# Kernel optimization log

Measured on AMD Instinct MI355X. Metric: run time of the kernel, lower is better.

The kernel has to match this reference:

```python
import jax, jax.numpy as jnp
import numpy as np

B, R, T, N = 32, 2, 128, 128
C_IN, C_OUT = 64, 64


def setup_inputs() -> dict:
    key = jax.random.key(0)
    k1, k2, k3 = jax.random.split(key, 3)
    x = jax.random.normal(k1, (B, C_IN, T, N), dtype=jnp.float32)
    # non-negative adjacency weights (degrees stay positive after +I)
    A = jax.random.uniform(k2, (B, R, T, N, N), dtype=jnp.float32)
    # 1x1 conv weight (out_channels*relation, in_channels) and bias
    W = jax.random.normal(k3, (R * C_OUT, C_IN), dtype=jnp.float32) * 0.02
    b = jnp.zeros((R * C_OUT,), dtype=jnp.float32)
    return {"x": x, "A": A, "W": W, "b": b}


def _normalized_laplacian_tilde(A):
    # A: (..., N, N). GCN-style: A~ = A + I, D~^{-1/2} A~ D~^{-1/2}
    n = A.shape[-1]
    A_t = A + jnp.eye(n, dtype=A.dtype)
    d = jax.lax.rsqrt(A_t.sum(axis=-1))  # (..., N)
    return A_t * d[..., :, None] * d[..., None, :]


def reference(x, A, W, b):
    # 1x1 Conv2d over (T, N): pointwise channel mix
    y = jnp.einsum('bctn,oc->botn', x, W) + b[None, :, None, None]
    y = y.reshape(B, R, C_OUT, T, N)
    # drop_edge is identity in eval mode; normalize each (b, r, t) adjacency
    A_norm = _normalized_laplacian_tilde(A)  # (B, R, T, N, N)
    # torch.bmm(x_r[:, :, t, :], A_rt_norm) summed over relations:
    # x_out[b,c,t,n] = sum_r sum_m y[b,r,c,t,m] * A_norm[b,r,t,m,n]
    x_out = jnp.einsum('brctm,brtmn->bctn', y, A_norm)
    return (x_out, A)
```

## Files before the change

### kernel.cpp

```cpp
#include <hip/hip_runtime.h>
#include <hip/hip_bf16.h>

#define TB 512

constexpr size_t XOUT_ELEMS = 32ull * 64 * 128 * 128;

typedef short bf16x8  __attribute__((ext_vector_type(8)));
typedef short short4v __attribute__((ext_vector_type(4)));
typedef float f32x4   __attribute__((ext_vector_type(4)));

static __device__ __forceinline__ short f2bf(float f) {
    __hip_bfloat16 hb = __float2bfloat16(f);
    return *reinterpret_cast<short*>(&hb);
}


__global__ __launch_bounds__(TB, 4)
void gcn_fused(const float* __restrict__ xg, const float* __restrict__ Ag,
               const float* __restrict__ Wg, const float* __restrict__ bg,
               float* __restrict__ outg)
{
    __shared__ float4 smem4[5120];
    char*  smem = (char*)smem4;
    float* dd   = (float*)smem;

    const int tid = threadIdx.x;
    const int w   = tid >> 6;
    const int l   = tid & 63;
    const int g   = l >> 5;
    const int h   = l & 31;
    const int l15 = l & 15;
    const int l4  = l >> 4;

    const int blk = blockIdx.x;
    const int b = blk >> 7, t = blk & 127;

    {
        float vv[4][4];
        #pragma unroll
        for (int i = 0; i < 4; ++i) {
            int c = 8*w + 4*g + i;
            f32x4 v = __builtin_nontemporal_load(
                (const f32x4*)(xg + ((size_t)(b*64 + c)*128 + t)*128 + 4*h));
            vv[i][0] = v[0]; vv[i][1] = v[1]; vv[i][2] = v[2]; vv[i][3] = v[3];
        }
        int po = w ^ (h & 7);
        #pragma unroll
        for (int e = 0; e < 4; ++e) {
            int n = 4*h + e;
            short4v pk;
            pk[0] = f2bf(vv[0][e]); pk[1] = f2bf(vv[1][e]);
            pk[2] = f2bf(vv[2][e]); pk[3] = f2bf(vv[3][e]);
            *(short4v*)(smem + n*128 + po*16 + 8*g) = pk;
        }
    }
    #pragma unroll
    for (int k2 = 0; k2 < 4; ++k2) {
        int q = tid + TB*k2;
        f32x4 v = ((const f32x4*)Wg)[q];
        int o = q >> 4, oct = (q >> 1) & 7, hf = q & 1;
        short4v pk;
        pk[0] = f2bf(v[0]); pk[1] = f2bf(v[1]); pk[2] = f2bf(v[2]); pk[3] = f2bf(v[3]);
        *(short4v*)(smem + 49152 + o*128 + (oct ^ (o & 7))*16 + hf*8) = pk;
    }
    float bia[8];
    #pragma unroll
    for (int ot = 0; ot < 8; ++ot) bia[ot] = bg[16*ot + l15];
    __syncthreads();

    {
        const int n    = 16*w + l15;
        const int keyx = (n >> 2) & 7;
        bf16x8 af0 = *(const bf16x8*)(smem + n*128 + ((0 + l4) ^ keyx)*16);
        bf16x8 af1 = *(const bf16x8*)(smem + n*128 + ((4 + l4) ^ keyx)*16);
        const int m0   = 16*w + 4*l4;
        const int pob  = m0 >> 3;
        const int keyw = l15 & 7;
        #pragma unroll
        for (int ot = 0; ot < 8; ++ot) {
            int o = 16*ot + l15;
            f32x4 acc = {0.f, 0.f, 0.f, 0.f};
            bf16x8 bf0 = *(const bf16x8*)(smem + 49152 + o*128 + ((0 + l4) ^ keyw)*16);
            bf16x8 bf1 = *(const bf16x8*)(smem + 49152 + o*128 + ((4 + l4) ^ keyw)*16);
            acc = __builtin_amdgcn_mfma_f32_16x16x32_bf16(af0, bf0, acc, 0, 0, 0);
            acc = __builtin_amdgcn_mfma_f32_16x16x32_bf16(af1, bf1, acc, 0, 0, 0);
            short4v pk;
            pk[0] = f2bf(acc[0] + bia[ot]); pk[1] = f2bf(acc[1] + bia[ot]);
            pk[2] = f2bf(acc[2] + bia[ot]); pk[3] = f2bf(acc[3] + bia[ot]);
            int po = pob ^ (o & 7);
            *(short4v*)(smem + 16384 + o*256 + po*16 + (m0 & 7)*2) = pk;
        }
    }
    __syncthreads();

    f32x4 tot[4] = {{0,0,0,0},{0,0,0,0},{0,0,0,0},{0,0,0,0}};

    #pragma unroll 1
    for (int r = 0; r < 2; ++r) {
        const size_t aoff = ((size_t)(b*2 + r)*128 + t) * 16384;
        const float* gA = Ag + aoff;
        float*       gO = outg + XOUT_ELEMS + aoff;

        {
            float vv[2][4][4];
            #pragma unroll
            for (int k = 0; k < 2; ++k)
                #pragma unroll
                for (int i = 0; i < 4; ++i) {
                    int m = 16*w + 8*k + 4*g + i;
                    f32x4 v = __builtin_nontemporal_load((const f32x4*)(gA + m*128 + 4*h));
                    __builtin_nontemporal_store(v, (f32x4*)(gO + m*128 + 4*h));
                    vv[k][i][0] = v[0]; vv[k][i][1] = v[1];
                    vv[k][i][2] = v[2]; vv[k][i][3] = v[3];
                }
            #pragma unroll
            for (int k = 0; k < 2; ++k)
                #pragma unroll
                for (int i = 0; i < 4; ++i) {
                    float s = vv[k][i][0] + vv[k][i][1] + vv[k][i][2] + vv[k][i][3];
                    s += __shfl_xor(s, 16); s += __shfl_xor(s, 8);
                    s += __shfl_xor(s, 4);  s += __shfl_xor(s, 2); s += __shfl_xor(s, 1);
                    float dv = rsqrtf(1.0f + s);
                    if (h == 4*w + 2*k + g) vv[k][i][i] += 1.0f;
                    vv[k][i][0] *= dv; vv[k][i][1] *= dv;
                    vv[k][i][2] *= dv; vv[k][i][3] *= dv;
                    if (h == 0) dd[16*w + 8*k + 4*g + i] = dv;
                }
            #pragma unroll
            for (int k = 0; k < 2; ++k) {
                int po = (2*w + k) ^ (h & 7);
                #pragma unroll
                for (int e = 0; e < 4; ++e) {
                    int n = 4*h + e;
                    short4v pk;
                    pk[0] = f2bf(vv[k][0][e]); pk[1] = f2bf(vv[k][1][e]);
                    pk[2] = f2bf(vv[k][2][e]); pk[3] = f2bf(vv[k][3][e]);
                    *(short4v*)(smem + 49152 + n*256 + po*16 + 8*g) = pk;
                }
            }
        }
        __syncthreads();

        {
            f32x4 acc[4] = {{0,0,0,0},{0,0,0,0},{0,0,0,0},{0,0,0,0}};
            const int n    = 16*w + l15;
            const int keyA = (n >> 2) & 7;
            #pragma unroll
            for (int s = 0; s < 4; ++s) {
                int octk = 4*s + l4;
                bf16x8 bfr = *(const bf16x8*)(smem + 49152 + n*256 + (octk ^ keyA)*16);
                #pragma unroll
                for (int ct = 0; ct < 4; ++ct) {
                    int o  = 64*r + 16*ct + l15;
                    bf16x8 afr = *(const bf16x8*)(smem + 16384 + o*256 + (octk ^ (o & 7))*16);
                    acc[ct] = __builtin_amdgcn_mfma_f32_16x16x32_bf16(afr, bfr, acc[ct], 0, 0, 0);
                }
            }
            float dn = dd[n];
            #pragma unroll
            for (int ct = 0; ct < 4; ++ct)
                #pragma unroll
                for (int j = 0; j < 4; ++j) tot[ct][j] += acc[ct][j] * dn;
        }
        __syncthreads();
    }

    #pragma unroll
    for (int ct = 0; ct < 4; ++ct)
        #pragma unroll
        for (int j = 0; j < 4; ++j) {
            int c = 16*ct + 4*l4 + j;
            int n = 16*w + l15;
            __builtin_nontemporal_store(tot[ct][j],
                &outg[((size_t)(b*64 + c)*128 + t)*128 + n]);
        }
}

extern "C" void kernel_launch(void* const* d_in, const int* in_sizes, int n_in,
                              void* d_out, int out_size, void* d_ws, size_t ws_size,
                              hipStream_t stream) {
    const float* x    = (const float*)d_in[0];
    const float* A    = (const float*)d_in[1];
    const float* W    = (const float*)d_in[2];
    const float* bias = (const float*)d_in[3];
    float* out = (float*)d_out;

    dim3 grid(32 * 128);
    dim3 block(TB);
    hipLaunchKernelGGL(gcn_fused, grid, block, 0, stream, x, A, W, bias, out);
}
```

Before: 236.4 us.

## Prefetch A tiles into registers and overlap loads with GEMM stages

Issues the global loads for x, W and the first adjacency slice together at kernel start, and prefetches the second relation's adjacency slice before the first relation's GEMM. Replaces __syncthreads with an LDS-only waitcnt plus s_barrier so outstanding global loads are not drained at each barrier. The relation loop is unrolled into explicit stages, and A/x loads drop the nontemporal hint. This is meant to hide global memory latency behind LDS work and MFMA, at the cost of higher register pressure under the 4-block launch bound.

```diff
diff --git a/kernel.cpp b/kernel.cpp
--- a/kernel.cpp
+++ b/kernel.cpp
@@ -14,6 +14,73 @@
     return *reinterpret_cast<short*>(&hb);
 }
 
+static __device__ __forceinline__ void lgkm_barrier() {
+    asm volatile("s_waitcnt lgkmcnt(0)" ::: "memory");
+    __builtin_amdgcn_s_barrier();
+    asm volatile("" ::: "memory");
+}
+
+
+static __device__ __forceinline__ void process_A(f32x4 (&av)[2][4], float* __restrict__ gO,
+                                                 char* smem, float* dd,
+                                                 int w, int g, int h) {
+    #pragma unroll
+    for (int k = 0; k < 2; ++k)
+        #pragma unroll
+        for (int i = 0; i < 4; ++i) {
+            int m = 16*w + 8*k + 4*g + i;
+            __builtin_nontemporal_store(av[k][i], (f32x4*)(gO + m*128 + 4*h));
+        }
+    #pragma unroll
+    for (int k = 0; k < 2; ++k)
+        #pragma unroll
+        for (int i = 0; i < 4; ++i) {
+            float s = av[k][i][0] + av[k][i][1] + av[k][i][2] + av[k][i][3];
+            s += __shfl_xor(s, 16); s += __shfl_xor(s, 8);
+            s += __shfl_xor(s, 4);  s += __shfl_xor(s, 2); s += __shfl_xor(s, 1);
+            float dv = rsqrtf(1.0f + s);
+            if (h == 4*w + 2*k + g) av[k][i][i] += 1.0f;
+            av[k][i][0] *= dv; av[k][i][1] *= dv;
+            av[k][i][2] *= dv; av[k][i][3] *= dv;
+            if (h == 0) dd[16*w + 8*k + 4*g + i] = dv;
+        }
+    #pragma unroll
+    for (int k = 0; k < 2; ++k) {
+        int po = (2*w + k) ^ (h & 7);
+        #pragma unroll
+        for (int e = 0; e < 4; ++e) {
+            int n = 4*h + e;
+            short4v pk;
+            pk[0] = f2bf(av[k][0][e]); pk[1] = f2bf(av[k][1][e]);
+            pk[2] = f2bf(av[k][2][e]); pk[3] = f2bf(av[k][3][e]);
+            *(short4v*)(smem + 49152 + n*256 + po*16 + 8*g) = pk;
+        }
+    }
+}
+
+static __device__ __forceinline__ void gemm2(int r, f32x4 (&tot)[4],
+                                             const char* smem, const float* dd,
+                                             int l15, int l4, int w) {
+    f32x4 acc[4] = {{0,0,0,0},{0,0,0,0},{0,0,0,0},{0,0,0,0}};
+    const int n    = 16*w + l15;
+    const int keyA = (n >> 2) & 7;
+    #pragma unroll
+    for (int s = 0; s < 4; ++s) {
+        int octk = 4*s + l4;
+        bf16x8 bfr = *(const bf16x8*)(smem + 49152 + n*256 + (octk ^ keyA)*16);
+        #pragma unroll
+        for (int ct = 0; ct < 4; ++ct) {
+            int o  = 64*r + 16*ct + l15;
+            bf16x8 afr = *(const bf16x8*)(smem + 16384 + o*256 + (octk ^ (o & 7))*16);
+            acc[ct] = __builtin_amdgcn_mfma_f32_16x16x32_bf16(afr, bfr, acc[ct], 0, 0, 0);
+        }
+    }
+    float dn = dd[n];
+    #pragma unroll
+    for (int ct = 0; ct < 4; ++ct)
+        #pragma unroll
+        for (int j = 0; j < 4; ++j) tot[ct][j] += acc[ct][j] * dn;
+}
 
 __global__ __launch_bounds__(TB, 4)
 void gcn_fused(const float* __restrict__ xg, const float* __restrict__ Ag,
@@ -35,38 +102,55 @@
     const int blk = blockIdx.x;
     const int b = blk >> 7, t = blk & 127;
 
+    const size_t aoff0 = ((size_t)(b*2 + 0)*128 + t) * 16384;
+    const size_t aoff1 = ((size_t)(b*2 + 1)*128 + t) * 16384;
+    const float* gA0 = Ag + aoff0;
+    const float* gA1 = Ag + aoff1;
+    float*       gO0 = outg + XOUT_ELEMS + aoff0;
+    float*       gO1 = outg + XOUT_ELEMS + aoff1;
+
+    f32x4 xr[4];
+    #pragma unroll
+    for (int i = 0; i < 4; ++i) {
+        int c = 8*w + 4*g + i;
+        xr[i] = *(const f32x4*)(xg + ((size_t)(b*64 + c)*128 + t)*128 + 4*h);
+    }
+    f32x4 wr[4];
+    #pragma unroll
+    for (int k2 = 0; k2 < 4; ++k2) wr[k2] = ((const f32x4*)Wg)[tid + TB*k2];
+    f32x4 av[2][4];
+    #pragma unroll
+    for (int k = 0; k < 2; ++k)
+        #pragma unroll
+        for (int i = 0; i < 4; ++i) {
+            int m = 16*w + 8*k + 4*g + i;
+            av[k][i] = *(const f32x4*)(gA0 + m*128 + 4*h);
+        }
+    float bia[8];
+    #pragma unroll
+    for (int ot = 0; ot < 8; ++ot) bia[ot] = bg[16*ot + l15];
+
     {
-        float vv[4][4];
-        #pragma unroll
-        for (int i = 0; i < 4; ++i) {
-            int c = 8*w + 4*g + i;
-            f32x4 v = __builtin_nontemporal_load(
-                (const f32x4*)(xg + ((size_t)(b*64 + c)*128 + t)*128 + 4*h));
-            vv[i][0] = v[0]; vv[i][1] = v[1]; vv[i][2] = v[2]; vv[i][3] = v[3];
-        }
         int po = w ^ (h & 7);
         #pragma unroll
         for (int e = 0; e < 4; ++e) {
             int n = 4*h + e;
             short4v pk;
-            pk[0] = f2bf(vv[0][e]); pk[1] = f2bf(vv[1][e]);
-            pk[2] = f2bf(vv[2][e]); pk[3] = f2bf(vv[3][e]);
+            pk[0] = f2bf(xr[0][e]); pk[1] = f2bf(xr[1][e]);
+            pk[2] = f2bf(xr[2][e]); pk[3] = f2bf(xr[3][e]);
             *(short4v*)(smem + n*128 + po*16 + 8*g) = pk;
         }
     }
     #pragma unroll
     for (int k2 = 0; k2 < 4; ++k2) {
         int q = tid + TB*k2;
-        f32x4 v = ((const f32x4*)Wg)[q];
         int o = q >> 4, oct = (q >> 1) & 7, hf = q & 1;
         short4v pk;
-        pk[0] = f2bf(v[0]); pk[1] = f2bf(v[1]); pk[2] = f2bf(v[2]); pk[3] = f2bf(v[3]);
+        pk[0] = f2bf(wr[k2][0]); pk[1] = f2bf(wr[k2][1]);
+        pk[2] = f2bf(wr[k2][2]); pk[3] = f2bf(wr[k2][3]);
         *(short4v*)(smem + 49152 + o*128 + (oct ^ (o & 7))*16 + hf*8) = pk;
     }
-    float bia[8];
-    #pragma unroll
-    for (int ot = 0; ot < 8; ++ot) bia[ot] = bg[16*ot + l15];
-    __syncthreads();
+    lgkm_barrier();
 
     {
         const int n    = 16*w + l15;
@@ -91,79 +175,25 @@
             *(short4v*)(smem + 16384 + o*256 + po*16 + (m0 & 7)*2) = pk;
         }
     }
-    __syncthreads();
+    lgkm_barrier();
 
     f32x4 tot[4] = {{0,0,0,0},{0,0,0,0},{0,0,0,0},{0,0,0,0}};
 
-    #pragma unroll 1
-    for (int r = 0; r < 2; ++r) {
-        const size_t aoff = ((size_t)(b*2 + r)*128 + t) * 16384;
-        const float* gA = Ag + aoff;
-        float*       gO = outg + XOUT_ELEMS + aoff;
-
-        {
-            float vv[2][4][4];
-            #pragma unroll
-            for (int k = 0; k < 2; ++k)
-                #pragma unroll
-                for (int i = 0; i < 4; ++i) {
-                    int m = 16*w + 8*k + 4*g + i;
-                    f32x4 v = __builtin_nontemporal_load((const f32x4*)(gA + m*128 + 4*h));
-                    __builtin_nontemporal_store(v, (f32x4*)(gO + m*128 + 4*h));
-                    vv[k][i][0] = v[0]; vv[k][i][1] = v[1];
-                    vv[k][i][2] = v[2]; vv[k][i][3] = v[3];
-                }
-            #pragma unroll
-            for (int k = 0; k < 2; ++k)
-                #pragma unroll
-                for (int i = 0; i < 4; ++i) {
-                    float s = vv[k][i][0] + vv[k][i][1] + vv[k][i][2] + vv[k][i][3];
-                    s += __shfl_xor(s, 16); s += __shfl_xor(s, 8);
-                    s += __shfl_xor(s, 4);  s += __shfl_xor(s, 2); s += __shfl_xor(s, 1);
-                    float dv = rsqrtf(1.0f + s);
-                    if (h == 4*w + 2*k + g) vv[k][i][i] += 1.0f;
-                    vv[k][i][0] *= dv; vv[k][i][1] *= dv;
-                    vv[k][i][2] *= dv; vv[k][i][3] *= dv;
-                    if (h == 0) dd[16*w + 8*k + 4*g + i] = dv;
-                }
-            #pragma unroll
-            for (int k = 0; k < 2; ++k) {
-                int po = (2*w + k) ^ (h & 7);
-                #pragma unroll
-                for (int e = 0; e < 4; ++e) {
-                    int n = 4*h + e;
-                    short4v pk;
-                    pk[0] = f2bf(vv[k][0][e]); pk[1] = f2bf(vv[k][1][e]);
-                    pk[2] = f2bf(vv[k][2][e]); pk[3] = f2bf(vv[k][3][e]);
-                    *(short4v*)(smem + 49152 + n*256 + po*16 + 8*g) = pk;
-                }
-            }
-        }
-        __syncthreads();
-
-        {
-            f32x4 acc[4] = {{0,0,0,0},{0,0,0,0},{0,0,0,0},{0,0,0,0}};
-            const int n    = 16*w + l15;
-            const int keyA = (n >> 2) & 7;
-            #pragma unroll
-            for (int s = 0; s < 4; ++s) {
-                int octk = 4*s + l4;
-                bf16x8 bfr = *(const bf16x8*)(smem + 49152 + n*256 + (octk ^ keyA)*16);
-                #pragma unroll
-                for (int ct = 0; ct < 4; ++ct) {
-                    int o  = 64*r + 16*ct + l15;
-                    bf16x8 afr = *(const bf16x8*)(smem + 16384 + o*256 + (octk ^ (o & 7))*16);
-                    acc[ct] = __builtin_amdgcn_mfma_f32_16x16x32_bf16(afr, bfr, acc[ct], 0, 0, 0);
-                }
-            }
-            float dn = dd[n];
-            #pragma unroll
-            for (int ct = 0; ct < 4; ++ct)
-                #pragma unroll
-                for (int j = 0; j < 4; ++j) tot[ct][j] += acc[ct][j] * dn;
-        }
-        __syncthreads();
-    }
+    process_A(av, gO0, smem, dd, w, g, h);
+    #pragma unroll
+    for (int k = 0; k < 2; ++k)
+        #pragma unroll
+        for (int i = 0; i < 4; ++i) {
+            int m = 16*w + 8*k + 4*g + i;
+            av[k][i] = *(const f32x4*)(gA1 + m*128 + 4*h);
+        }
+    lgkm_barrier();
+    gemm2(0, tot, smem, dd, l15, l4, w);
+    lgkm_barrier();
+
+    process_A(av, gO1, smem, dd, w, g, h);
+    lgkm_barrier();
+    gemm2(1, tot, smem, dd, l15, l4, w);
 
     #pragma unroll
     for (int ct = 0; ct < 4; ++ct)
```

After: 260.4 us. 10.2% more time.

## Split adjacency staging into halves to shrink LDS and raise occupancy

Applied to the files above, without the earlier changes.

The per-relation adjacency tile is now staged and multiplied in two 64-row halves that reuse the x staging region. This cuts shared memory from about 80KB to about 48KB, and launch bounds are raised to target 6 blocks per CU. W and bias are no longer staged in LDS; each wave loads them straight from global memory and converts them to bf16 in registers. The cost is extra barriers per relation, redundant global W reads in every block, and possible register pressure under the tighter launch bound.

```diff
diff --git a/kernel.cpp b/kernel.cpp
--- a/kernel.cpp
+++ b/kernel.cpp
@@ -15,14 +15,66 @@
 }
 
 
-__global__ __launch_bounds__(TB, 4)
+static __device__ __forceinline__ void stage_half(const float* __restrict__ gA,
+                                                  float* __restrict__ gO, int hf,
+                                                  char* smem, float* dd,
+                                                  int w, int g, int h) {
+    const int mb = 64*hf + 8*w + 4*g;
+    f32x4 av[4];
+    #pragma unroll
+    for (int i = 0; i < 4; ++i)
+        av[i] = __builtin_nontemporal_load((const f32x4*)(gA + (size_t)(mb+i)*128 + 4*h));
+    #pragma unroll
+    for (int i = 0; i < 4; ++i)
+        __builtin_nontemporal_store(av[i], (f32x4*)(gO + (size_t)(mb+i)*128 + 4*h));
+    #pragma unroll
+    for (int i = 0; i < 4; ++i) {
+        float s = av[i][0] + av[i][1] + av[i][2] + av[i][3];
+        s += __shfl_xor(s, 16); s += __shfl_xor(s, 8);
+        s += __shfl_xor(s, 4);  s += __shfl_xor(s, 2); s += __shfl_xor(s, 1);
+        float dv = rsqrtf(1.0f + s);
+        if (h == 16*hf + 2*w + g) av[i][i] += 1.0f;
+        av[i][0] *= dv; av[i][1] *= dv; av[i][2] *= dv; av[i][3] *= dv;
+        if (h == 0) dd[mb + i] = dv;
+    }
+    const int po = w ^ (h & 7);
+    #pragma unroll
+    for (int e = 0; e < 4; ++e) {
+        int n = 4*h + e;
+        short4v pk;
+        pk[0] = f2bf(av[0][e]); pk[1] = f2bf(av[1][e]);
+        pk[2] = f2bf(av[2][e]); pk[3] = f2bf(av[3][e]);
+        *(short4v*)(smem + n*128 + po*16 + 8*g) = pk;
+    }
+}
+
+static __device__ __forceinline__ void gemm2_half(int r, int hf, f32x4 (&acc)[4],
+                                                  const char* smem,
+                                                  int l15, int l4, int w) {
+    const int n    = 16*w + l15;
+    const int keyA = (n >> 2) & 7;
+    #pragma unroll
+    for (int s = 0; s < 2; ++s) {
+        int ol = 4*s + l4;
+        bf16x8 bfr = *(const bf16x8*)(smem + n*128 + (ol ^ keyA)*16);
+        int og = 8*hf + 4*s + l4;
+        #pragma unroll
+        for (int ct = 0; ct < 4; ++ct) {
+            int o  = 64*r + 16*ct + l15;
+            bf16x8 afr = *(const bf16x8*)(smem + 16384 + o*256 + (og ^ (o & 7))*16);
+            acc[ct] = __builtin_amdgcn_mfma_f32_16x16x32_bf16(afr, bfr, acc[ct], 0, 0, 0);
+        }
+    }
+}
+
+__global__ __launch_bounds__(TB, 6)
 void gcn_fused(const float* __restrict__ xg, const float* __restrict__ Ag,
                const float* __restrict__ Wg, const float* __restrict__ bg,
                float* __restrict__ outg)
 {
-    __shared__ float4 smem4[5120];
+    __shared__ float4 smem4[3104];
     char*  smem = (char*)smem4;
-    float* dd   = (float*)smem;
+    float* dd   = (float*)(smem + 49152);
 
     const int tid = threadIdx.x;
     const int w   = tid >> 6;
@@ -36,36 +88,23 @@
     const int b = blk >> 7, t = blk & 127;
 
     {
-        float vv[4][4];
+        f32x4 xr[4];
         #pragma unroll
         for (int i = 0; i < 4; ++i) {
             int c = 8*w + 4*g + i;
-            f32x4 v = __builtin_nontemporal_load(
+            xr[i] = __builtin_nontemporal_load(
                 (const f32x4*)(xg + ((size_t)(b*64 + c)*128 + t)*128 + 4*h));
-            vv[i][0] = v[0]; vv[i][1] = v[1]; vv[i][2] = v[2]; vv[i][3] = v[3];
         }
         int po = w ^ (h & 7);
         #pragma unroll
         for (int e = 0; e < 4; ++e) {
             int n = 4*h + e;
             short4v pk;
-            pk[0] = f2bf(vv[0][e]); pk[1] = f2bf(vv[1][e]);
-            pk[2] = f2bf(vv[2][e]); pk[3] = f2bf(vv[3][e]);
+            pk[0] = f2bf(xr[0][e]); pk[1] = f2bf(xr[1][e]);
+            pk[2] = f2bf(xr[2][e]); pk[3] = f2bf(xr[3][e]);
             *(short4v*)(smem + n*128 + po*16 + 8*g) = pk;
         }
     }
-    #pragma unroll
-    for (int k2 = 0; k2 < 4; ++k2) {
-        int q = tid + TB*k2;
-        f32x4 v = ((const f32x4*)Wg)[q];
-        int o = q >> 4, oct = (q >> 1) & 7, hf = q & 1;
-        short4v pk;
-        pk[0] = f2bf(v[0]); pk[1] = f2bf(v[1]); pk[2] = f2bf(v[2]); pk[3] = f2bf(v[3]);
-        *(short4v*)(smem + 49152 + o*128 + (oct ^ (o & 7))*16 + hf*8) = pk;
-    }
-    float bia[8];
-    #pragma unroll
-    for (int ot = 0; ot < 8; ++ot) bia[ot] = bg[16*ot + l15];
     __syncthreads();
 
     {
@@ -73,20 +112,27 @@
         const int keyx = (n >> 2) & 7;
         bf16x8 af0 = *(const bf16x8*)(smem + n*128 + ((0 + l4) ^ keyx)*16);
         bf16x8 af1 = *(const bf16x8*)(smem + n*128 + ((4 + l4) ^ keyx)*16);
-        const int m0   = 16*w + 4*l4;
-        const int pob  = m0 >> 3;
-        const int keyw = l15 & 7;
+        const int m0  = 16*w + 4*l4;
+        const int pob = m0 >> 3;
         #pragma unroll
         for (int ot = 0; ot < 8; ++ot) {
             int o = 16*ot + l15;
+            const f32x4* wp = (const f32x4*)(Wg + o*64 + 8*l4);
+            f32x4 w0a = wp[0], w0b = wp[1];
+            const f32x4* wq = (const f32x4*)(Wg + o*64 + 32 + 8*l4);
+            f32x4 w1a = wq[0], w1b = wq[1];
+            float bb = bg[o];
+            bf16x8 bf0, bf1;
+            bf0[0]=f2bf(w0a[0]); bf0[1]=f2bf(w0a[1]); bf0[2]=f2bf(w0a[2]); bf0[3]=f2bf(w0a[3]);
+            bf0[4]=f2bf(w0b[0]); bf0[5]=f2bf(w0b[1]); bf0[6]=f2bf(w0b[2]); bf0[7]=f2bf(w0b[3]);
+            bf1[0]=f2bf(w1a[0]); bf1[1]=f2bf(w1a[1]); bf1[2]=f2bf(w1a[2]); bf1[3]=f2bf(w1a[3]);
+            bf1[4]=f2bf(w1b[0]); bf1[5]=f2bf(w1b[1]); bf1[6]=f2bf(w1b[2]); bf1[7]=f2bf(w1b[3]);
             f32x4 acc = {0.f, 0.f, 0.f, 0.f};
-            bf16x8 bf0 = *(const bf16x8*)(smem + 49152 + o*128 + ((0 + l4) ^ keyw)*16);
-            bf16x8 bf1 = *(const bf16x8*)(smem + 49152 + o*128 + ((4 + l4) ^ keyw)*16);
             acc = __builtin_amdgcn_mfma_f32_16x16x32_bf16(af0, bf0, acc, 0, 0, 0);
             acc = __builtin_amdgcn_mfma_f32_16x16x32_bf16(af1, bf1, acc, 0, 0, 0);
             short4v pk;
-            pk[0] = f2bf(acc[0] + bia[ot]); pk[1] = f2bf(acc[1] + bia[ot]);
-            pk[2] = f2bf(acc[2] + bia[ot]); pk[3] = f2bf(acc[3] + bia[ot]);
+            pk[0] = f2bf(acc[0] + bb); pk[1] = f2bf(acc[1] + bb);
+            pk[2] = f2bf(acc[2] + bb); pk[3] = f2bf(acc[3] + bb);
             int po = pob ^ (o & 7);
             *(short4v*)(smem + 16384 + o*256 + po*16 + (m0 & 7)*2) = pk;
         }
@@ -101,67 +147,21 @@
         const float* gA = Ag + aoff;
         float*       gO = outg + XOUT_ELEMS + aoff;
 
-        {
-            float vv[2][4][4];
+        f32x4 acc[4] = {{0,0,0,0},{0,0,0,0},{0,0,0,0},{0,0,0,0}};
+
+        stage_half(gA, gO, 0, smem, dd, w, g, h);
+        __syncthreads();
+        gemm2_half(r, 0, acc, smem, l15, l4, w);
+        __syncthreads();
+        stage_half(gA, gO, 1, smem, dd, w, g, h);
+        __syncthreads();
+        gemm2_half(r, 1, acc, smem, l15, l4, w);
+
+        float dn = dd[16*w + l15];
+        #pragma unroll
+        for (int ct = 0; ct < 4; ++ct)
             #pragma unroll
-            for (int k = 0; k < 2; ++k)
-                #pragma unroll
-                for (int i = 0; i < 4; ++i) {
-                    int m = 16*w + 8*k + 4*g + i;
-                    f32x4 v = __builtin_nontemporal_load((const f32x4*)(gA + m*128 + 4*h));
-                    __builtin_nontemporal_store(v, (f32x4*)(gO + m*128 + 4*h));
-                    vv[k][i][0] = v[0]; vv[k][i][1] = v[1];
-                    vv[k][i][2] = v[2]; vv[k][i][3] = v[3];
-                }
-            #pragma unroll
-            for (int k = 0; k < 2; ++k)
-                #pragma unroll
-                for (int i = 0; i < 4; ++i) {
-                    float s = vv[k][i][0] + vv[k][i][1] + vv[k][i][2] + vv[k][i][3];
-                    s += __shfl_xor(s, 16); s += __shfl_xor(s, 8);
-                    s += __shfl_xor(s, 4);  s += __shfl_xor(s, 2); s += __shfl_xor(s, 1);
-                    float dv = rsqrtf(1.0f + s);
-                    if (h == 4*w + 2*k + g) vv[k][i][i] += 1.0f;
-                    vv[k][i][0] *= dv; vv[k][i][1] *= dv;
-                    vv[k][i][2] *= dv; vv[k][i][3] *= dv;
-                    if (h == 0) dd[16*w + 8*k + 4*g + i] = dv;
-                }
-            #pragma unroll
-            for (int k = 0; k < 2; ++k) {
-                int po = (2*w + k) ^ (h & 7);
-                #pragma unroll
-                for (int e = 0; e < 4; ++e) {
-                    int n = 4*h + e;
-                    short4v pk;
-                    pk[0] = f2bf(vv[k][0][e]); pk[1] = f2bf(vv[k][1][e]);
-                    pk[2] = f2bf(vv[k][2][e]); pk[3] = f2bf(vv[k][3][e]);
-                    *(short4v*)(smem + 49152 + n*256 + po*16 + 8*g) = pk;
-                }
-            }
-        }
-        __syncthreads();
-
-        {
-            f32x4 acc[4] = {{0,0,0,0},{0,0,0,0},{0,0,0,0},{0,0,0,0}};
-            const int n    = 16*w + l15;
-            const int keyA = (n >> 2) & 7;
-            #pragma unroll
-            for (int s = 0; s < 4; ++s) {
-                int octk = 4*s + l4;
-                bf16x8 bfr = *(const bf16x8*)(smem + 49152 + n*256 + (octk ^ keyA)*16);
-                #pragma unroll
-                for (int ct = 0; ct < 4; ++ct) {
-                    int o  = 64*r + 16*ct + l15;
-                    bf16x8 afr = *(const bf16x8*)(smem + 16384 + o*256 + (octk ^ (o & 7))*16);
-                    acc[ct] = __builtin_amdgcn_mfma_f32_16x16x32_bf16(afr, bfr, acc[ct], 0, 0, 0);
-                }
-            }
-            float dn = dd[n];
-            #pragma unroll
-            for (int ct = 0; ct < 4; ++ct)
-                #pragma unroll
-                for (int j = 0; j < 4; ++j) tot[ct][j] += acc[ct][j] * dn;
-        }
+            for (int j = 0; j < 4; ++j) tot[ct][j] += acc[ct][j] * dn;
         __syncthreads();
     }
 
```

Measured after the change: 265.0 us. 1.12x slower.
